# Kernel optimization log

Measured on AMD Instinct MI355X. Metric: run time of the kernel, lower is better.

## Reference

```python
import jax, jax.numpy as jnp
import numpy as np

H = 512      # hidden_size
E = 300      # embed_size
V = 50257    # output_size / vocab
B = 64       # batch
S = 128      # src_len
NEG = -1e10


def setup_inputs() -> dict:
    key = jax.random.key(0)
    ks = jax.random.split(key, 12)
    inp = {
        "input_ids": jax.random.randint(ks[0], (B,), 0, V),
        "hidden": jax.random.normal(ks[1], (B, H), jnp.float32),
        "encoder_outputs": jax.random.normal(ks[2], (S, B, 2 * H), jnp.float32),
        "mask": jax.random.randint(ks[3], (B, S), 0, 2).astype(jnp.int32),
        # parameters
        "emb_table": jax.random.normal(ks[4], (V, E), jnp.float32) * 0.02,
        "W_attn": jax.random.normal(ks[5], (H, 3 * H), jnp.float32) * 0.02,
        "b_attn": jnp.zeros((H,), jnp.float32),
        "v_w": jax.random.normal(ks[6], (1, H), jnp.float32) * 0.02,
        "W_ih": jax.random.normal(ks[7], (3 * H, 2 * H + E), jnp.float32) * 0.02,
        "W_hh": jax.random.normal(ks[8], (3 * H, H), jnp.float32) * 0.02,
        "b_ih": jnp.zeros((3 * H,), jnp.float32),
        "b_hh": jnp.zeros((3 * H,), jnp.float32),
        "W_out": jax.random.normal(ks[9], (V, 3 * H + E), jnp.float32) * 0.02,
        "b_out": jnp.zeros((V,), jnp.float32),
    }
    return inp


def reference(input_ids, hidden, encoder_outputs, mask,
              emb_table, W_attn, b_attn, v_w,
              W_ih, W_hh, b_ih, b_hh, W_out, b_out):
    # embedding lookup (dropout prob = 0 -> identity)
    embedded = emb_table[input_ids]                       # [B, E]

    # Bahdanau attention
    enc_b = jnp.transpose(encoder_outputs, (1, 0, 2))     # [B, S, 2H]
    hid_rep = jnp.broadcast_to(hidden[:, None, :], (hidden.shape[0], enc_b.shape[1], hidden.shape[1]))
    energy = jnp.tanh(jnp.concatenate([hid_rep, enc_b], axis=2) @ W_attn.T + b_attn)  # [B, S, H]
    scores = jnp.einsum('bsh,h->bs', energy, v_w[0])      # [B, S]
    scores = jnp.where(mask == 0, NEG, scores)
    a = jax.nn.softmax(scores, axis=1)                    # [B, S]

    # context vector
    weighted = jnp.einsum('bs,bse->be', a, enc_b)         # [B, 2H]

    # single-step GRU (PyTorch gate order: r, z, n)
    x = jnp.concatenate([embedded, weighted], axis=1)     # [B, E + 2H]
    gx = x @ W_ih.T + b_ih                                # [B, 3H]
    gh = hidden @ W_hh.T + b_hh                           # [B, 3H]
    h = hidden.shape[1]
    r = jax.nn.sigmoid(gx[:, :h] + gh[:, :h])
    z = jax.nn.sigmoid(gx[:, h:2*h] + gh[:, h:2*h])
    n = jnp.tanh(gx[:, 2*h:] + r * gh[:, 2*h:])
    h_new = (1.0 - z) * n + z * hidden                    # [B, H]

    # output projection
    prediction = jnp.concatenate([h_new, weighted, embedded], axis=1) @ W_out.T + b_out  # [B, V]
    return prediction, h_new, a
```

## Files before the change

kernel.cpp:

```cpp
#include <hip/hip_runtime.h>

typedef unsigned short ushort_t;
typedef short bf16x8 __attribute__((ext_vector_type(8)));
typedef float f32x4 __attribute__((ext_vector_type(4)));

#define B_ 64
#define H_ 512
#define E_ 300
#define V_ 50257
#define S_ 128

#define HNEW_OFS ((size_t)64 * 50257)
#define A_OFS    ((size_t)64 * 50257 + 64 * 512)

__device__ __forceinline__ unsigned short f2b(float f) {
  unsigned int u = __builtin_bit_cast(unsigned int, f);
  u = u + 0x7FFFu + ((u >> 16) & 1u);
  return (unsigned short)(u >> 16);
}
__device__ __forceinline__ float fast_tanh(float x) {
  x = fminf(15.f, fmaxf(-15.f, x));
  float e = __expf(-2.f * x);
  return (1.f - e) / (1.f + e);
}
__device__ __forceinline__ float fast_sigmoid(float x) {
  return 1.f / (1.f + __expf(-x));
}

template <int DT> struct Raw4;
template <> struct Raw4<0> {
  ushort4 v;
  __device__ static Raw4 zero() { return {make_ushort4(0, 0, 0, 0)}; }
};
template <> struct Raw4<1> {
  float4 v;
  __device__ static Raw4 zero() { return {make_float4(0.f, 0.f, 0.f, 0.f)}; }
};
template <int DT>
__device__ __forceinline__ Raw4<DT> ld_raw(const void* p, size_t off);
template <>
__device__ __forceinline__ Raw4<0> ld_raw<0>(const void* p, size_t off) {
  return {*(const ushort4*)((const ushort_t*)p + off)};
}
template <>
__device__ __forceinline__ Raw4<1> ld_raw<1>(const void* p, size_t off) {
  return {*(const float4*)((const float*)p + off)};
}
template <int DT>
__device__ __forceinline__ ushort4 to_b4(Raw4<DT> r);
template <>
__device__ __forceinline__ ushort4 to_b4<0>(Raw4<0> r) { return r.v; }
template <>
__device__ __forceinline__ ushort4 to_b4<1>(Raw4<1> r) {
  return make_ushort4(f2b(r.v.x), f2b(r.v.y), f2b(r.v.z), f2b(r.v.w));
}

template <int DTA, int DTW>
__global__ __launch_bounds__(256) void gemm_tile(
    const void* __restrict__ A, int lda,
    const void* __restrict__ W, int ldw, int wofs,
    const float* __restrict__ bias,
    float* __restrict__ C, int ldc,
    int M, int N, int K)
{
  __shared__ ushort_t sA[64 * 40];
  __shared__ ushort_t sB[64 * 40];
  const int tid = threadIdx.x;
  const int n0 = blockIdx.x * 64, m0 = blockIdx.y * 64;
  const int wave = tid >> 6, lane = tid & 63, quad = lane >> 4, l16 = lane & 15;

  f32x4 acc[4];
  #pragma unroll
  for (int i = 0; i < 4; ++i) acc[i] = (f32x4){0.f, 0.f, 0.f, 0.f};

  Raw4<DTA> ra[2];
  Raw4<DTW> rb[2];
  auto fetch = [&](int kt) {
    #pragma unroll
    for (int i = 0; i < 2; ++i) {
      int g = tid + i * 256;
      int row = g >> 3, gc = (g & 7) << 2;
      int gk = kt * 32 + gc;
      int ar = m0 + row, wr = n0 + row;
      ra[i] = Raw4<DTA>::zero();
      rb[i] = Raw4<DTW>::zero();
      if (gk < K && ar < M) ra[i] = ld_raw<DTA>(A, (size_t)ar * lda + gk);
      if (gk < K && wr < N) rb[i] = ld_raw<DTW>(W, (size_t)wr * ldw + wofs + gk);
    }
  };
  const int ksteps = (K + 31) >> 5;
  fetch(0);
  for (int kt = 0; kt < ksteps; ++kt) {
    #pragma unroll
    for (int i = 0; i < 2; ++i) {
      int g = tid + i * 256;
      int row = g >> 3, gc = (g & 7) << 2;
      *(ushort4*)(sA + row * 40 + gc) = to_b4<DTA>(ra[i]);
      *(ushort4*)(sB + row * 40 + gc) = to_b4<DTW>(rb[i]);
    }
    __syncthreads();
    if (kt + 1 < ksteps) fetch(kt + 1);
    bf16x8 af = *(const bf16x8*)(sA + (wave * 16 + l16) * 40 + quad * 8);
    #pragma unroll
    for (int nt = 0; nt < 4; ++nt) {
      bf16x8 bfr = *(const bf16x8*)(sB + (nt * 16 + l16) * 40 + quad * 8);
      acc[nt] = __builtin_amdgcn_mfma_f32_16x16x32_bf16(af, bfr, acc[nt], 0, 0, 0);
    }
    __syncthreads();
  }
  #pragma unroll
  for (int nt = 0; nt < 4; ++nt) {
    #pragma unroll
    for (int reg = 0; reg < 4; ++reg) {
      int row = m0 + wave * 16 + quad * 4 + reg;
      int col = n0 + nt * 16 + l16;
      if (row < M && col < N)
        C[(size_t)row * ldc + col] = acc[nt][reg] + bias[col];
    }
  }
}

__global__ __launch_bounds__(256) void attn_scores(
    const float* __restrict__ enc,
    const float* __restrict__ Wattn,
    const float* __restrict__ Gh,
    const float* __restrict__ vw,
    float* __restrict__ scores_part)
{
  __shared__ ushort_t sA[64 * 40];
  __shared__ ushort_t sB[64 * 40];
  const int tid = threadIdx.x;
  const int n0 = blockIdx.x * 64, m0 = blockIdx.y * 64;
  const int wave = tid >> 6, lane = tid & 63, quad = lane >> 4, l16 = lane & 15;

  f32x4 acc[4];
  #pragma unroll
  for (int i = 0; i < 4; ++i) acc[i] = (f32x4){0.f, 0.f, 0.f, 0.f};

  float4 ra[2], rb[2];
  auto fetch = [&](int kt) {
    #pragma unroll
    for (int i = 0; i < 2; ++i) {
      int g = tid + i * 256;
      int row = g >> 3, gc = (g & 7) << 2;
      int gk = kt * 32 + gc;
      ra[i] = *(const float4*)(enc + (size_t)(m0 + row) * 1024 + gk);
      rb[i] = *(const float4*)(Wattn + (size_t)(n0 + row) * 1536 + 512 + gk);
    }
  };
  fetch(0);
  for (int kt = 0; kt < 32; ++kt) {
    #pragma unroll
    for (int i = 0; i < 2; ++i) {
      int g = tid + i * 256;
      int row = g >> 3, gc = (g & 7) << 2;
      *(ushort4*)(sA + row * 40 + gc) =
          make_ushort4(f2b(ra[i].x), f2b(ra[i].y), f2b(ra[i].z), f2b(ra[i].w));
      *(ushort4*)(sB + row * 40 + gc) =
          make_ushort4(f2b(rb[i].x), f2b(rb[i].y), f2b(rb[i].z), f2b(rb[i].w));
    }
    __syncthreads();
    if (kt + 1 < 32) fetch(kt + 1);
    bf16x8 af = *(const bf16x8*)(sA + (wave * 16 + l16) * 40 + quad * 8);
    #pragma unroll
    for (int nt = 0; nt < 4; ++nt) {
      bf16x8 bfr = *(const bf16x8*)(sB + (nt * 16 + l16) * 40 + quad * 8);
      acc[nt] = __builtin_amdgcn_mfma_f32_16x16x32_bf16(af, bfr, acc[nt], 0, 0, 0);
    }
    __syncthreads();
  }
  float psum[4] = {0.f, 0.f, 0.f, 0.f};
  #pragma unroll
  for (int nt = 0; nt < 4; ++nt) {
    int h = n0 + nt * 16 + l16;
    float vh = vw[h];
    #pragma unroll
    for (int reg = 0; reg < 4; ++reg) {
      int r = m0 + wave * 16 + quad * 4 + reg;
      int b = r & 63;
      float e = acc[nt][reg] + Gh[b * 512 + h];
      psum[reg] += vh * fast_tanh(e);
    }
  }
  #pragma unroll
  for (int reg = 0; reg < 4; ++reg) {
    float p = psum[reg];
    p += __shfl_xor(p, 1);
    p += __shfl_xor(p, 2);
    p += __shfl_xor(p, 4);
    p += __shfl_xor(p, 8);
    if (l16 == 0) {
      int r = m0 + wave * 16 + quad * 4 + reg;
      scores_part[blockIdx.x * 8192 + r] = p;
    }
  }
}

__global__ __launch_bounds__(256) void softmax_ctx(
    const float* __restrict__ scores_part,
    const int* __restrict__ mask,
    const float* __restrict__ enc,
    const float* __restrict__ emb,
    const int* __restrict__ ids,
    float* __restrict__ out,
    ushort_t* __restrict__ x,
    ushort_t* __restrict__ xo)
{
  __shared__ float sc[128];
  __shared__ float red[128];
  const int b = blockIdx.x;
  const int tid = threadIdx.x;

  if (tid < 128) {
    float s = 0.f;
    #pragma unroll
    for (int nb = 0; nb < 8; ++nb) s += scores_part[nb * 8192 + tid * 64 + b];
    if (mask[b * 128 + tid] == 0) s = -1e10f;
    sc[tid] = s;
    red[tid] = s;
  }
  __syncthreads();
  for (int off = 64; off > 0; off >>= 1) {
    if (tid < off) red[tid] = fmaxf(red[tid], red[tid + off]);
    __syncthreads();
  }
  float m = red[0];
  __syncthreads();
  if (tid < 128) {
    float e = __expf(sc[tid] - m);
    sc[tid] = e;
    red[tid] = e;
  }
  __syncthreads();
  for (int off = 64; off > 0; off >>= 1) {
    if (tid < off) red[tid] += red[tid + off];
    __syncthreads();
  }
  float inv = 1.f / red[0];
  if (tid < 128) {
    float av = sc[tid] * inv;
    sc[tid] = av;
    out[A_OFS + b * 128 + tid] = av;
  }
  __syncthreads();

  {
    int e0 = tid * 4;
    float a0 = 0.f, a1 = 0.f, a2 = 0.f, a3 = 0.f;
    for (int s = 0; s < 128; ++s) {
      float as = sc[s];
      float4 ev = *(const float4*)(enc + (size_t)(s * 64 + b) * 1024 + e0);
      a0 += as * ev.x;
      a1 += as * ev.y;
      a2 += as * ev.z;
      a3 += as * ev.w;
    }
    ushort4 wb = make_ushort4(f2b(a0), f2b(a1), f2b(a2), f2b(a3));
    *(ushort4*)(x + b * 1344 + 300 + e0) = wb;
    *(ushort4*)(xo + b * 1856 + 512 + e0) = wb;
  }

  int rid = ids[b];
  for (int e = tid; e < 300; e += 256) {
    ushort_t h = f2b(emb[(size_t)rid * 300 + e]);
    x[b * 1344 + e] = h;
    xo[b * 1856 + 1536 + e] = h;
  }
  if (tid < 20) {
    x[b * 1344 + 1324 + tid] = 0;
    xo[b * 1856 + 1836 + tid] = 0;
  }
}

__global__ __launch_bounds__(256) void gru_pointwise(
    const float* __restrict__ gx,
    const float* __restrict__ gh,
    const float* __restrict__ hidden,
    float* __restrict__ out,
    ushort_t* __restrict__ xo)
{
  int i = blockIdx.x * 256 + threadIdx.x;
  int b = i >> 9, h = i & 511;
  float r = fast_sigmoid(gx[b * 1536 + h] + gh[b * 1536 + h]);
  float z = fast_sigmoid(gx[b * 1536 + 512 + h] + gh[b * 1536 + 512 + h]);
  float n = fast_tanh(gx[b * 1536 + 1024 + h] + r * gh[b * 1536 + 1024 + h]);
  float hp = hidden[b * 512 + h];
  float hn = (1.f - z) * n + z * hp;
  out[HNEW_OFS + b * 512 + h] = hn;
  xo[b * 1856 + h] = f2b(hn);
}

__global__ __launch_bounds__(256) void out_proj2(
    const ushort_t* __restrict__ Xo,
    const float* __restrict__ Wout,
    const float* __restrict__ bout,
    float* __restrict__ pred)
{
  __shared__ ushort_t sA[2][64 * 40];
  const int tid = threadIdx.x;
  const int n0 = blockIdx.x * 64;
  const int wave = tid >> 6, lane = tid & 63, quad = lane >> 4, l16 = lane & 15;

  const int col = n0 + wave * 16 + l16;
  const int colc = (col < V_) ? col : 0;
  const float* pB = Wout + (size_t)colc * 1836;

  const int arow = tid >> 2;
  const int acol = (tid & 3) * 8;
  const ushort_t* pA = Xo + (size_t)arow * 1856 + acol;
  ushort_t* sAw0 = &sA[0][arow * 40 + acol];
  ushort_t* sAw1 = &sA[1][arow * 40 + acol];

  f32x4 acc[4];
  #pragma unroll
  for (int i = 0; i < 4; ++i) acc[i] = (f32x4){0.f, 0.f, 0.f, 0.f};

  float4 b0a, b0b, b1a, b1b;
  auto ldB = [&](int kt, float4& va, float4& vb) {
    int k0 = kt * 32 + quad * 8;
    int ka = (k0 < 1832) ? k0 : 1832;
    int kb = (k0 + 4 < 1832) ? (k0 + 4) : 1832;
    va = *(const float4*)(pB + ka);
    vb = *(const float4*)(pB + kb);
  };
  auto packB = [](float4 a, float4 b) {
    bf16x8 r;
    r[0] = (short)f2b(a.x); r[1] = (short)f2b(a.y);
    r[2] = (short)f2b(a.z); r[3] = (short)f2b(a.w);
    r[4] = (short)f2b(b.x); r[5] = (short)f2b(b.y);
    r[6] = (short)f2b(b.z); r[7] = (short)f2b(b.w);
    return r;
  };
  auto mfma4 = [&](const ushort_t* base, bf16x8 bf) {
    #pragma unroll
    for (int mt = 0; mt < 4; ++mt) {
      bf16x8 af = *(const bf16x8*)(base + (mt * 16 + l16) * 40 + quad * 8);
      acc[mt] = __builtin_amdgcn_mfma_f32_16x16x32_bf16(af, bf, acc[mt], 0, 0, 0);
    }
  };

  ldB(0, b0a, b0b);
  bf16x8 aReg = *(const bf16x8*)(pA);
  *(bf16x8*)sAw0 = aReg;
  aReg = *(const bf16x8*)(pA + 32);
  ldB(1, b1a, b1b);
  __syncthreads();

  #pragma unroll 1
  for (int kt = 0; kt < 58; kt += 2) {
    {
      if (kt + 1 < 58) *(bf16x8*)sAw1 = aReg;
      bf16x8 bf = packB(b0a, b0b);
      if (kt + 2 < 58) {
        ldB(kt + 2, b0a, b0b);
        aReg = *(const bf16x8*)(pA + (size_t)(kt + 2) * 32);
      }
      mfma4(&sA[0][0], bf);
      __syncthreads();
    }
    {
      if (kt + 3 < 58) *(bf16x8*)sAw0 = aReg;
      bf16x8 bf = packB(b1a, b1b);
      if (kt + 3 < 58) {
        ldB(kt + 3, b1a, b1b);
        aReg = *(const bf16x8*)(pA + (size_t)(kt + 3) * 32);
      }
      mfma4(&sA[1][0], bf);
      __syncthreads();
    }
  }

  if (col < V_) {
    float bc = bout[col];
    #pragma unroll
    for (int mt = 0; mt < 4; ++mt) {
      #pragma unroll
      for (int reg = 0; reg < 4; ++reg) {
        int prow = mt * 16 + quad * 4 + reg;
        pred[(size_t)prow * V_ + col] = acc[mt][reg] + bc;
      }
    }
  }
}

extern "C" void kernel_launch(void* const* d_in, const int* in_sizes, int n_in,
                              void* d_out, int out_size, void* d_ws, size_t ws_size,
                              hipStream_t stream) {
  const int*   ids    = (const int*)d_in[0];
  const float* hidden = (const float*)d_in[1];
  const float* enc    = (const float*)d_in[2];
  const int*   mask   = (const int*)d_in[3];
  const float* emb    = (const float*)d_in[4];
  const float* Wattn  = (const float*)d_in[5];
  const float* battn  = (const float*)d_in[6];
  const float* vw     = (const float*)d_in[7];
  const float* Wih    = (const float*)d_in[8];
  const float* Whh    = (const float*)d_in[9];
  const float* bih    = (const float*)d_in[10];
  const float* bhh    = (const float*)d_in[11];
  const float* Wout   = (const float*)d_in[12];
  const float* bout   = (const float*)d_in[13];
  float* out = (float*)d_out;

  char* ws = (char*)d_ws;
  float*    scores_part = (float*)(ws + 0);
  float*    Gh          = (float*)(ws + 262144);
  float*    gx          = (float*)(ws + 393216);
  float*    gh          = (float*)(ws + 786432);
  ushort_t* x           = (ushort_t*)(ws + 1179648);
  ushort_t* xo          = (ushort_t*)(ws + 1351680);

  gemm_tile<1, 1><<<dim3(8, 1), 256, 0, stream>>>(
      hidden, 512, Wattn, 1536, 0, battn, Gh, 512, 64, 512, 512);

  attn_scores<<<dim3(8, 128), 256, 0, stream>>>(enc, Wattn, Gh, vw, scores_part);

  softmax_ctx<<<64, 256, 0, stream>>>(scores_part, mask, enc, emb, ids, out, x, xo);

  gemm_tile<0, 1><<<dim3(24, 1), 256, 0, stream>>>(
      x, 1344, Wih, 1324, 0, bih, gx, 1536, 64, 1536, 1324);
  gemm_tile<1, 1><<<dim3(24, 1), 256, 0, stream>>>(
      hidden, 512, Whh, 512, 0, bhh, gh, 1536, 64, 1536, 512);

  gru_pointwise<<<128, 256, 0, stream>>>(gx, gh, hidden, out, xo);

  out_proj2<<<786, 256, 0, stream>>>(xo, Wout, bout, out);
}
```

Baseline: 727.4 us.

## Double-buffer LDS in GEMM tiles and merge GRU gate GEMMs into one launch

Converts the gemm_tile and attn_scores main loops to double-buffered shared memory, so the next tile is staged while MFMAs run on the current one. This drops one barrier per k-step. The separate gx and gh GEMM launches are merged into a single kernel whose grid y-dimension selects the input/weight pair, saving a launch and letting both run concurrently. The bf16 conversion now uses the library intrinsic. Costs are doubled LDS use per block and some extra branching in the merged kernel. The dominant output projection is untouched, so the effect on total time is likely small.

```diff
diff --git a/kernel.cpp b/kernel.cpp
--- a/kernel.cpp
+++ b/kernel.cpp
@@ -1,4 +1,5 @@
 #include <hip/hip_runtime.h>
+#include <hip/hip_bf16.h>
 
 typedef unsigned short ushort_t;
 typedef short bf16x8 __attribute__((ext_vector_type(8)));
@@ -13,10 +14,8 @@
 #define HNEW_OFS ((size_t)64 * 50257)
 #define A_OFS    ((size_t)64 * 50257 + 64 * 512)
 
-__device__ __forceinline__ unsigned short f2b(float f) {
-  unsigned int u = __builtin_bit_cast(unsigned int, f);
-  u = u + 0x7FFFu + ((u >> 16) & 1u);
-  return (unsigned short)(u >> 16);
+__device__ __forceinline__ ushort_t f2b(float f) {
+  return __builtin_bit_cast(ushort_t, __float2bfloat16(f));
 }
 __device__ __forceinline__ float fast_tanh(float x) {
   x = fminf(15.f, fmaxf(-15.f, x));
@@ -63,8 +62,8 @@
     float* __restrict__ C, int ldc,
     int M, int N, int K)
 {
-  __shared__ ushort_t sA[64 * 40];
-  __shared__ ushort_t sB[64 * 40];
+  __shared__ ushort_t sA[2][64 * 40];
+  __shared__ ushort_t sB[2][64 * 40];
   const int tid = threadIdx.x;
   const int n0 = blockIdx.x * 64, m0 = blockIdx.y * 64;
   const int wave = tid >> 6, lane = tid & 63, quad = lane >> 4, l16 = lane & 15;
@@ -88,22 +87,27 @@
       if (gk < K && wr < N) rb[i] = ld_raw<DTW>(W, (size_t)wr * ldw + wofs + gk);
     }
   };
-  const int ksteps = (K + 31) >> 5;
-  fetch(0);
-  for (int kt = 0; kt < ksteps; ++kt) {
+  auto stage = [&](int buf) {
     #pragma unroll
     for (int i = 0; i < 2; ++i) {
       int g = tid + i * 256;
       int row = g >> 3, gc = (g & 7) << 2;
-      *(ushort4*)(sA + row * 40 + gc) = to_b4<DTA>(ra[i]);
-      *(ushort4*)(sB + row * 40 + gc) = to_b4<DTW>(rb[i]);
-    }
-    __syncthreads();
-    if (kt + 1 < ksteps) fetch(kt + 1);
-    bf16x8 af = *(const bf16x8*)(sA + (wave * 16 + l16) * 40 + quad * 8);
+      *(ushort4*)(sA[buf] + row * 40 + gc) = to_b4<DTA>(ra[i]);
+      *(ushort4*)(sB[buf] + row * 40 + gc) = to_b4<DTW>(rb[i]);
+    }
+  };
+  const int ksteps = (K + 31) >> 5;
+  fetch(0);
+  stage(0);
+  if (ksteps > 1) fetch(1);
+  __syncthreads();
+  for (int kt = 0; kt < ksteps; ++kt) {
+    if (kt + 1 < ksteps) stage((kt + 1) & 1);
+    if (kt + 2 < ksteps) fetch(kt + 2);
+    bf16x8 af = *(const bf16x8*)(sA[kt & 1] + (wave * 16 + l16) * 40 + quad * 8);
     #pragma unroll
     for (int nt = 0; nt < 4; ++nt) {
-      bf16x8 bfr = *(const bf16x8*)(sB + (nt * 16 + l16) * 40 + quad * 8);
+      bf16x8 bfr = *(const bf16x8*)(sB[kt & 1] + (nt * 16 + l16) * 40 + quad * 8);
       acc[nt] = __builtin_amdgcn_mfma_f32_16x16x32_bf16(af, bfr, acc[nt], 0, 0, 0);
     }
     __syncthreads();
@@ -127,8 +131,8 @@
     const float* __restrict__ vw,
     float* __restrict__ scores_part)
 {
-  __shared__ ushort_t sA[64 * 40];
-  __shared__ ushort_t sB[64 * 40];
+  __shared__ ushort_t sA[2][64 * 40];
+  __shared__ ushort_t sB[2][64 * 40];
   const int tid = threadIdx.x;
   const int n0 = blockIdx.x * 64, m0 = blockIdx.y * 64;
   const int wave = tid >> 6, lane = tid & 63, quad = lane >> 4, l16 = lane & 15;
@@ -148,23 +152,28 @@
       rb[i] = *(const float4*)(Wattn + (size_t)(n0 + row) * 1536 + 512 + gk);
     }
   };
-  fetch(0);
-  for (int kt = 0; kt < 32; ++kt) {
+  auto stage = [&](int buf) {
     #pragma unroll
     for (int i = 0; i < 2; ++i) {
       int g = tid + i * 256;
       int row = g >> 3, gc = (g & 7) << 2;
-      *(ushort4*)(sA + row * 40 + gc) =
+      *(ushort4*)(sA[buf] + row * 40 + gc) =
           make_ushort4(f2b(ra[i].x), f2b(ra[i].y), f2b(ra[i].z), f2b(ra[i].w));
-      *(ushort4*)(sB + row * 40 + gc) =
+      *(ushort4*)(sB[buf] + row * 40 + gc) =
           make_ushort4(f2b(rb[i].x), f2b(rb[i].y), f2b(rb[i].z), f2b(rb[i].w));
     }
-    __syncthreads();
-    if (kt + 1 < 32) fetch(kt + 1);
-    bf16x8 af = *(const bf16x8*)(sA + (wave * 16 + l16) * 40 + quad * 8);
+  };
+  fetch(0);
+  stage(0);
+  fetch(1);
+  __syncthreads();
+  for (int kt = 0; kt < 32; ++kt) {
+    if (kt + 1 < 32) stage((kt + 1) & 1);
+    if (kt + 2 < 32) fetch(kt + 2);
+    bf16x8 af = *(const bf16x8*)(sA[kt & 1] + (wave * 16 + l16) * 40 + quad * 8);
     #pragma unroll
     for (int nt = 0; nt < 4; ++nt) {
-      bf16x8 bfr = *(const bf16x8*)(sB + (nt * 16 + l16) * 40 + quad * 8);
+      bf16x8 bfr = *(const bf16x8*)(sB[kt & 1] + (nt * 16 + l16) * 40 + quad * 8);
       acc[nt] = __builtin_amdgcn_mfma_f32_16x16x32_bf16(af, bfr, acc[nt], 0, 0, 0);
     }
     __syncthreads();
@@ -269,6 +278,89 @@
   if (tid < 20) {
     x[b * 1344 + 1324 + tid] = 0;
     xo[b * 1856 + 1836 + tid] = 0;
+  }
+}
+
+__global__ __launch_bounds__(256) void gemm_gxgh(
+    const ushort_t* __restrict__ xb,
+    const float* __restrict__ hidden,
+    const float* __restrict__ Wih,
+    const float* __restrict__ Whh,
+    const float* __restrict__ bih,
+    const float* __restrict__ bhh,
+    float* __restrict__ gxo,
+    float* __restrict__ gho)
+{
+  __shared__ ushort_t sA[2][64 * 40];
+  __shared__ ushort_t sB[2][64 * 40];
+  const int tid = threadIdx.x;
+  const bool isGh = blockIdx.y != 0;
+  const int n0 = blockIdx.x * 64;
+  const int K = isGh ? 512 : 1324;
+  const float* W = isGh ? Whh : Wih;
+  const float* bias = isGh ? bhh : bih;
+  float* C = isGh ? gho : gxo;
+  const int wave = tid >> 6, lane = tid & 63, quad = lane >> 4, l16 = lane & 15;
+
+  f32x4 acc[4];
+  #pragma unroll
+  for (int i = 0; i < 4; ++i) acc[i] = (f32x4){0.f, 0.f, 0.f, 0.f};
+
+  ushort4 rab[2];
+  float4 raf[2];
+  float4 rb[2];
+  auto fetch = [&](int kt) {
+    #pragma unroll
+    for (int i = 0; i < 2; ++i) {
+      int g = tid + i * 256;
+      int row = g >> 3, gc = (g & 7) << 2;
+      int gk = kt * 32 + gc;
+      if (isGh) {
+        raf[i] = *(const float4*)(hidden + (size_t)row * 512 + gk);
+      } else {
+        rab[i] = *(const ushort4*)(xb + (size_t)row * 1344 + gk);
+      }
+      rb[i] = make_float4(0.f, 0.f, 0.f, 0.f);
+      if (gk < K) rb[i] = *(const float4*)(W + (size_t)(n0 + row) * K + gk);
+    }
+  };
+  auto stage = [&](int buf) {
+    #pragma unroll
+    for (int i = 0; i < 2; ++i) {
+      int g = tid + i * 256;
+      int row = g >> 3, gc = (g & 7) << 2;
+      ushort4 a = isGh
+          ? make_ushort4(f2b(raf[i].x), f2b(raf[i].y), f2b(raf[i].z), f2b(raf[i].w))
+          : rab[i];
+      *(ushort4*)(sA[buf] + row * 40 + gc) = a;
+      *(ushort4*)(sB[buf] + row * 40 + gc) =
+          make_ushort4(f2b(rb[i].x), f2b(rb[i].y), f2b(rb[i].z), f2b(rb[i].w));
+    }
+  };
+  const int ksteps = isGh ? 16 : 42;
+  fetch(0);
+  stage(0);
+  fetch(1);
+  __syncthreads();
+  for (int kt = 0; kt < ksteps; ++kt) {
+    if (kt + 1 < ksteps) stage((kt + 1) & 1);
+    if (kt + 2 < ksteps) fetch(kt + 2);
+    bf16x8 af = *(const bf16x8*)(sA[kt & 1] + (wave * 16 + l16) * 40 + quad * 8);
+    #pragma unroll
+    for (int nt = 0; nt < 4; ++nt) {
+      bf16x8 bfr = *(const bf16x8*)(sB[kt & 1] + (nt * 16 + l16) * 40 + quad * 8);
+      acc[nt] = __builtin_amdgcn_mfma_f32_16x16x32_bf16(af, bfr, acc[nt], 0, 0, 0);
+    }
+    __syncthreads();
+  }
+  #pragma unroll
+  for (int nt = 0; nt < 4; ++nt) {
+    #pragma unroll
+    for (int reg = 0; reg < 4; ++reg) {
+      int row = wave * 16 + quad * 4 + reg;
+      int col = n0 + nt * 16 + l16;
+      C[(size_t)row * 1536 + col] = acc[nt][reg] + bias[col];
+    }
   }
 }
 
@@ -417,10 +509,8 @@
 
   softmax_ctx<<<64, 256, 0, stream>>>(scores_part, mask, enc, emb, ids, out, x, xo);
 
-  gemm_tile<0, 1><<<dim3(24, 1), 256, 0, stream>>>(
-      x, 1344, Wih, 1324, 0, bih, gx, 1536, 64, 1536, 1324);
-  gemm_tile<1, 1><<<dim3(24, 1), 256, 0, stream>>>(
-      hidden, 512, Whh, 512, 0, bhh, gh, 1536, 64, 1536, 512);
+  gemm_gxgh<<<dim3(24, 2), 256, 0, stream>>>(
+      x, hidden, Wih, Whh, bih, bhh, gx, gh);
 
   gru_pointwise<<<128, 256, 0, stream>>>(gx, gh, hidden, out, xo);
 
```

Measured after the change: 714.8 us. No clear change (-1.7%).
